# Kernel tuning notes

Measured on AMD Instinct MI355X. Metric: run time of the kernel, lower is better.

The kernel has to match this reference:

```python
import jax, jax.numpy as jnp
import numpy as np

BETA = 1.0  # config.beta
B, G, K, E2 = 1024, 512, 128, 128


def setup_inputs() -> dict:
    key = jax.random.key(0)
    k1, k2, k3, k4, k5 = jax.random.split(key, 5)
    s = 0.05
    return {
        "images": jax.random.normal(k1, (B, G), dtype=jnp.float32),
        "wimg": jax.random.normal(k2, (G, K), dtype=jnp.float32) * s,    # project.weight.T
        "wrec": jax.random.normal(k3, (K, E2), dtype=jnp.float32) * s,   # rec.weight.T
        "wrec2": jax.random.normal(k4, (K + 1, E2), dtype=jnp.float32) * s,  # rec2.weight.T
        "wimg2": jax.random.normal(k5, (G, K, K + 1), dtype=jnp.float32) * s,  # img2.weight.T.reshape(K+1,K,G).T
    }


def _soft_assign(x, codes):
    # x: [B, D], codes: [D, C] -> softmax over C of -beta * mean_D (x - codes)^2
    xh = -jnp.mean((x[:, :, None] - codes[None]) ** 2, axis=1) * BETA  # [B, C]
    return jax.nn.softmax(xh, axis=-1)


def reference(images, wimg, wrec, wrec2, wimg2):
    # ---- encode ----
    xp = _soft_assign(images, wimg)            # [B, K]
    lat = xp @ wrec                            # [B, E2]
    xp = _soft_assign(lat, wrec.T)             # [B, K] (codes are wrec.T: [E2, K])
    idx = jnp.argmax(xp, axis=-1)              # [B] hard component
    xwimg = jnp.transpose(wimg2[:, idx, :], (1, 0, 2))   # [B, G, K+1]
    base = wimg[:, idx].T[:, :, None]                     # [B, G, 1]
    xd = images[:, :, None] - base - xwimg                # [B, G, K+1]
    xh2 = -jnp.mean(xd ** 2, axis=1) * BETA               # [B, K+1]
    xp2 = jax.nn.softmax(xh2, axis=-1)
    lat2 = xp2 @ wrec2                                    # [B, E2]
    # ---- decode (ret='rec', n_step>=1) ----
    xp_d = _soft_assign(lat, wrec.T)           # [B, K]
    xp2_d = _soft_assign(lat2, wrec2.T)        # [B, K+1]
    wimgg = wimg[:, :, None] + wimg2           # [G, K, K+1]
    # tensordot(xp_d[:, :, None]*xp2_d[:, None, :], wimgg.permute(1,2,0), 2)
    xrec = jnp.einsum('bk,bj,gkj->bg', xp_d, xp2_d, wimgg)  # [B, G]
    # ---- loss ----
    loss = jnp.mean((xrec - images) ** 2, axis=-1)  # [B]
    return loss
```

## Files before the change

### kernel.cpp

```cpp
#include <hip/hip_runtime.h>

#define B_    1024
#define G_    512
#define K_    128
#define J_    129
#define JP_   132
#define E2_   128
#define KK_   16512
#define KK2_  16896
#define KKE2_ 17024
#define KKP_  17408
#define SPLITS 16
#define KCHUNK 1088
#define BK_   32
#define KSTEPS 34
#define GS_   8

using short8 = __attribute__((ext_vector_type(8))) short;
using f32x4  = __attribute__((ext_vector_type(4))) float;

__device__ __forceinline__ float bf2f(unsigned short h){
  return __uint_as_float(((unsigned int)h) << 16);
}
__device__ __forceinline__ unsigned short f2bf(float f){
  unsigned int u = __float_as_uint(f);
  u += 0x7fffu + ((u >> 16) & 1u);
  return (unsigned short)(u >> 16);
}

#define GLOAD16(gptr, ldst) __builtin_amdgcn_global_load_lds( \
    (const __attribute__((address_space(1))) unsigned int*)(gptr), \
    (__attribute__((address_space(3))) unsigned int*)(ldst), 16, 0, 0)

__device__ __forceinline__ float blockSum512(float v, float* red, int t){
  #pragma unroll
  for (int off = 32; off > 0; off >>= 1) v += __shfl_down(v, off);
  __syncthreads();
  if ((t & 63) == 0) red[t >> 6] = v;
  __syncthreads();
  float r = ((red[0] + red[1]) + (red[2] + red[3]))
          + ((red[4] + red[5]) + (red[6] + red[7]));
  __syncthreads();
  return r;
}

__device__ __forceinline__ void blockSoftmaxMS512(float x, bool act,
    float* redm, float* reds, int t, float& mo, float& so){
  float m = x, s = act ? 1.f : 0.f;
  #pragma unroll
  for (int off = 32; off > 0; off >>= 1){
    float om = __shfl_down(m, off);
    float os = __shfl_down(s, off);
    float nm = fmaxf(m, om);
    s = s*__expf(m - nm) + os*__expf(om - nm);
    m = nm;
  }
  __syncthreads();
  if ((t & 63) == 0){ redm[t >> 6] = m; reds[t >> 6] = s; }
  __syncthreads();
  float gm = redm[0], gsv = reds[0];
  #pragma unroll
  for (int w = 1; w < 8; w++){
    float om = redm[w], os = reds[w];
    float nm = fmaxf(gm, om);
    gsv = gsv*__expf(gm - nm) + os*__expf(om - nm);
    gm = nm;
  }
  mo = gm; so = gsv;
}

__device__ __forceinline__ int blockSoftmaxMSI512(float x, int idx, bool act,
    float* redm, float* reds, int* redi, int t, float& mo, float& so){
  float m = x, s = act ? 1.f : 0.f; int i = idx;
  #pragma unroll
  for (int off = 32; off > 0; off >>= 1){
    float om = __shfl_down(m, off);
    float os = __shfl_down(s, off);
    int   oi = __shfl_down(i, off);
    bool take = (om > m) || (om == m && oi < i);
    float nm = fmaxf(m, om);
    s = s*__expf(m - nm) + os*__expf(om - nm);
    i = take ? oi : i;
    m = nm;
  }
  __syncthreads();
  if ((t & 63) == 0){ redm[t >> 6] = m; reds[t >> 6] = s; redi[t >> 6] = i; }
  __syncthreads();
  float gm = redm[0], gsv = reds[0]; int gi = redi[0];
  #pragma unroll
  for (int w = 1; w < 8; w++){
    float om = redm[w], os = reds[w]; int oi = redi[w];
    bool take = (om > gm) || (om == gm && oi < gi);
    float nm = fmaxf(gm, om);
    gsv = gsv*__expf(gm - nm) + os*__expf(om - nm);
    gi = take ? oi : gi;
    gm = nm;
  }
  mo = gm; so = gsv;
  return gi;
}

__global__ __launch_bounds__(1024) void norms_kernel(
    const float* __restrict__ wimg, const float* __restrict__ wrec,
    const float* __restrict__ wrec2, float* __restrict__ c1norm,
    float* __restrict__ w3norm, float* __restrict__ w6norm,
    float* __restrict__ wrecT, float* __restrict__ wrec2T){
  int t = threadIdx.x;
  if (blockIdx.x == 0){
    __shared__ float red[8][128];
    int k = t & 127, sl = t >> 7;
    float s = 0.f;
    int g0 = sl * (G_/8);
    for (int g = g0; g < g0 + G_/8; g++){
      float v = wimg[g*K_ + k]; s += v*v;
    }
    red[sl][k] = s;
    __syncthreads();
    if (t < 128){
      float r = 0.f;
      #pragma unroll
      for (int i = 0; i < 8; i++) r += red[i][t];
      c1norm[t] = r;
    }
  } else if (blockIdx.x == 1){
    int wave = t >> 6, lane = t & 63;
    for (int k = wave; k < K_; k += 16){
      float v0 = wrec[k*E2_ + lane], v1 = wrec[k*E2_ + 64 + lane];
      float s = v0*v0 + v1*v1;
      #pragma unroll
      for (int off = 32; off > 0; off >>= 1) s += __shfl_down(s, off);
      if (lane == 0) w3norm[k] = s;
    }
  } else if (blockIdx.x == 2){
    int wave = t >> 6, lane = t & 63;
    for (int j = wave; j < J_; j += 16){
      float v0 = wrec2[j*E2_ + lane], v1 = wrec2[j*E2_ + 64 + lane];
      float s = v0*v0 + v1*v1;
      #pragma unroll
      for (int off = 32; off > 0; off >>= 1) s += __shfl_down(s, off);
      if (lane == 0) w6norm[j] = s;
    }
  } else if (blockIdx.x == 3){
    for (int n = t; n < K_*E2_; n += 1024){
      int k = n >> 7, e = n & 127;
      wrecT[e*K_ + k] = wrec[n];
    }
  } else {
    for (int n = t; n < J_*E2_; n += 1024){
      int j = n >> 7, e = n & 127;
      wrec2T[e*J_ + j] = wrec2[n];
    }
  }
}

__global__ __launch_bounds__(128) void tables_part_kernel(
    const float* __restrict__ wimg2, const float* __restrict__ wimg,
    float* __restrict__ sqp, float* __restrict__ crp,
    unsigned short* __restrict__ W2){
  int n  = blockIdx.x * 128 + threadIdx.x;
  int gs = blockIdx.y;
  int k = n / J_;
  int w2i = n + 3*k;
  float s0=0,s1=0,s2=0,s3=0, c0=0,c1=0,c2=0,c3=0;
  int gbase = gs * (G_/GS_);
  #pragma unroll 2
  for (int g = gbase; g < gbase + G_/GS_; g += 4){
    float w0 = wimg2[(size_t)(g  )*KK_ + n];
    float w1 = wimg2[(size_t)(g+1)*KK_ + n];
    float w2 = wimg2[(size_t)(g+2)*KK_ + n];
    float w3 = wimg2[(size_t)(g+3)*KK_ + n];
    W2[(size_t)(g  )*KKP_ + w2i] = f2bf(w0);
    W2[(size_t)(g+1)*KKP_ + w2i] = f2bf(w1);
    W2[(size_t)(g+2)*KKP_ + w2i] = f2bf(w2);
    W2[(size_t)(g+3)*KKP_ + w2i] = f2bf(w3);
    s0 += w0*w0; s1 += w1*w1; s2 += w2*w2; s3 += w3*w3;
    c0 += wimg[(g  )*K_ + k]*w0;
    c1 += wimg[(g+1)*K_ + k]*w1;
    c2 += wimg[(g+2)*K_ + k]*w2;
    c3 += wimg[(g+3)*K_ + k]*w3;
  }
  sqp[(size_t)gs*KK_ + n] = (s0+s1)+(s2+s3);
  crp[(size_t)gs*KK_ + n] = (c0+c1)+(c2+c3);
}
__global__ __launch_bounds__(128) void tables_reduce_kernel(
    const float* __restrict__ sqp, const float* __restrict__ crp,
    float* __restrict__ sq2, float* __restrict__ cross){
  int n = blockIdx.x * 128 + threadIdx.x;
  float s = 0.f, c = 0.f;
  #pragma unroll
  for (int gs = 0; gs < GS_; gs++){
    s += sqp[(size_t)gs*KK_ + n];
    c += crp[(size_t)gs*KK_ + n];
  }
  sq2[n] = s; cross[n] = c;
}

__global__ __launch_bounds__(128) void w2tail_kernel(
    const float* __restrict__ wimg, unsigned short* __restrict__ W2){
  int g = blockIdx.x, t = threadIdx.x;
  unsigned short* dst = W2 + (size_t)g * KKP_;
  dst[KK2_ + t]        = f2bf(wimg[g*K_ + t]);
  dst[KKE2_ + t]       = 0;
  dst[KKE2_ + 128 + t] = 0;
  dst[KKE2_ + 256 + t] = 0;
  dst[t*JP_ + 129] = 0;
  dst[t*JP_ + 130] = 0;
  dst[t*JP_ + 131] = 0;
}

__global__ __launch_bounds__(512, 8) void encdec_kernel(
    const float* __restrict__ img,  const float* __restrict__ wimg,
    const float* __restrict__ wrec, const float* __restrict__ wrec2,
    const float* __restrict__ wrecT, const float* __restrict__ wrec2T,
    const unsigned short* __restrict__ W2,
    const float* __restrict__ c1norm, const float* __restrict__ w3norm,
    const float* __restrict__ w6norm, const float* __restrict__ sq2,
    const float* __restrict__ cross, unsigned short* __restrict__ Rm){
  __shared__ __align__(16) float simg[G_];
  __shared__ float sp[K_];
  __shared__ float sqv[J_];
  __shared__ float slat[E2_];
  __shared__ float sd1[K_];
  __shared__ __align__(16) float sh16[16][128];
  __shared__ float sh4[4][K_];
  __shared__ float xtra[2];
  __shared__ float redm[8], reds[8];
  __shared__ int   redi[8];

  int t = threadIdx.x;
  int b = blockIdx.x;
  int tt = t & 127, q = t >> 7;
  int ll = t & 31, gq = t >> 5;

  simg[t] = img[b*G_ + t];
  __syncthreads();
  float a0 = simg[t];
  float imgnorm = blockSum512(a0*a0, redm, t);

  {
    float p0=0,p1=0,p2=0,p3=0;
    int g0 = gq * 32;
    #pragma unroll 4
    for (int g = g0; g < g0 + 32; g++){
      float4 wv = *(const float4*)(wimg + g*K_ + 4*ll);
      float sv = simg[g];
      p0 += sv*wv.x; p1 += sv*wv.y; p2 += sv*wv.z; p3 += sv*wv.w;
    }
    float4 st = {p0, p1, p2, p3};
    *(float4*)&sh16[gq][4*ll] = st;
  }
  __syncthreads();
  float xh1 = -3e38f, d1 = 0.f;
  if (t < 128){
    #pragma unroll
    for (int i = 0; i < 16; i++) d1 += sh16[i][t];
    sd1[t] = d1;
    xh1 = -(imgnorm - 2.f*d1 + c1norm[t]) * (1.f/512.f);
  }
  float m1, s1;
  blockSoftmaxMS512(xh1, t < 128, redm, reds, t, m1, s1);
  if (t < 128) sp[t] = __expf(xh1 - m1) / s1;
  __syncthreads();

  {
    float l0=0,l1=0;
    int k0 = q * 32;
    for (int k = k0; k < k0 + 32; k += 2){
      l0 += sp[k  ] * wrec[(k  )*E2_ + tt];
      l1 += sp[k+1] * wrec[(k+1)*E2_ + tt];
    }
    sh4[q][tt] = l0 + l1;
  }
  __syncthreads();
  float lat = (sh4[0][tt] + sh4[1][tt]) + (sh4[2][tt] + sh4[3][tt]);
  if (q == 0) slat[tt] = lat;
  float latnorm = blockSum512((q == 0) ? lat*lat : 0.f, redm, t);

  {
    float l0=0,l1=0;
    int e0 = q * 32;
    const float* rT = wrecT + tt;
    for (int e = e0; e < e0 + 32; e += 2){
      l0 += slat[e  ] * rT[(e  )*K_];
      l1 += slat[e+1] * rT[(e+1)*K_];
    }
    sh4[q][tt] = l0 + l1;
  }
  __syncthreads();
  float xh3 = -3e38f;
  if (t < 128){
    float d3 = (sh4[0][t] + sh4[1][t]) + (sh4[2][t] + sh4[3][t]);
    xh3 = -(latnorm - 2.f*d3 + w3norm[t]) * (1.f/128.f);
  }
  float m3, s3;
  int idxb = blockSoftmaxMSI512(xh3, tt, t < 128, redm, reds, redi, t, m3, s3);
  if (t < 128) sp[t] = __expf(xh3 - m3) / s3;
  float dsq = imgnorm - 2.f*sd1[idxb] + c1norm[idxb];

  {
    const unsigned short* Wb = W2 + (size_t)idxb * JP_ + 4*ll;
    float p0=0,p1=0,p2=0,p3=0;
    int g0 = gq * 32;
    #pragma unroll 4
    for (int g = g0; g < g0 + 32; g++){
      uint2 wv = *(const uint2*)(Wb + (size_t)g*KKP_);
      float sv = simg[g];
      p0 += sv * __uint_as_float(wv.x << 16);
      p1 += sv * __uint_as_float(wv.x & 0xffff0000u);
      p2 += sv * __uint_as_float(wv.y << 16);
      p3 += sv * __uint_as_float(wv.y & 0xffff0000u);
    }
    float4 st = {p0, p1, p2, p3};
    *(float4*)&sh16[gq][4*ll] = st;
  }
  if (t < 64){
    const unsigned short* Wb8 = W2 + (size_t)idxb * JP_ + 128;
    float s = 0.f;
    #pragma unroll
    for (int m = 0; m < 8; m++){
      int g = t + 64*m;
      s += simg[g] * bf2f(Wb8[(size_t)g * KKP_]);
    }
    #pragma unroll
    for (int off = 32; off > 0; off >>= 1) s += __shfl_down(s, off);
    if (t == 0) xtra[0] = s;
  }
  __syncthreads();
  float xh2 = -3e38f;
  if (t < J_){
    float di;
    if (t < 128){
      di = 0.f;
      #pragma unroll
      for (int i = 0; i < 16; i++) di += sh16[i][t];
    } else di = xtra[0];
    int nb = idxb*J_ + t;
    xh2 = -(dsq - 2.f*(di - cross[nb]) + sq2[nb]) * (1.f/512.f);
  }
  float m2, s2;
  blockSoftmaxMS512(xh2, t < J_, redm, reds, t, m2, s2);
  if (t < J_) sqv[t] = __expf(xh2 - m2) / s2;
  __syncthreads();

  {
    float lv = 0.f;
    int j0 = (q == 0) ? 0 : (q*32 + 1);
    int j1 = q*32 + 33;
    for (int j = j0; j < j1; j++)
      lv += sqv[j] * wrec2[j*E2_ + tt];
    sh4[q][tt] = lv;
  }
  __syncthreads();
  float lat2 = (sh4[0][tt] + sh4[1][tt]) + (sh4[2][tt] + sh4[3][tt]);
  if (q == 0) slat[tt] = lat2;
  float l2n = blockSum512((q == 0) ? lat2*lat2 : 0.f, redm, t);

  {
    float l0=0,l1=0;
    int e0 = q * 32;
    const float* rT = wrec2T + tt;
    for (int e = e0; e < e0 + 32; e += 2){
      l0 += slat[e  ] * rT[(e  )*J_];
      l1 += slat[e+1] * rT[(e+1)*J_];
    }
    sh4[q][tt] = l0 + l1;
  }
  if (t < 64){
    float s = slat[t]*wrec2T[t*J_ + 128] + slat[t+64]*wrec2T[(t+64)*J_ + 128];
    #pragma unroll
    for (int off = 32; off > 0; off >>= 1) s += __shfl_down(s, off);
    if (t == 0) xtra[1] = s;
  }
  __syncthreads();
  float xh6 = -3e38f;
  if (t < J_){
    float d6 = (t < 128) ? ((sh4[0][t] + sh4[1][t]) + (sh4[2][t] + sh4[3][t])) : xtra[1];
    xh6 = -(l2n - 2.f*d6 + w6norm[t]) * (1.f/128.f);
  }
  float m6, s6;
  blockSoftmaxMS512(xh6, t < J_, redm, reds, t, m6, s6);
  if (t < J_) sqv[t] = __expf(xh6 - m6) / s6;
  __syncthreads();

  unsigned short* Rrow = Rm + (size_t)b * KKP_;
  int k = t / JP_;
  int j = t - k*JP_;
  for (int kk = t; kk < KKP_; kk += 512){
    float v = 0.f;
    if (kk < KK2_){
      if (j < J_) v = sp[k] * sqv[j];
    } else if (kk < KKE2_) v = sp[kk - KK2_];
    Rrow[kk] = f2bf(v);
    j += 116;
    if (j >= JP_){ j -= JP_; k += 4; } else k += 3;
  }
}

__global__ __launch_bounds__(256) void gemm_kernel(
    const unsigned short* __restrict__ Rm, const unsigned short* __restrict__ W2,
    float* __restrict__ part){
  __shared__ __align__(16) unsigned int lds[4096];
  unsigned int* lA = lds;
  unsigned int* lB = lds + 2048;
  auto lA3 = (__attribute__((address_space(3))) unsigned int*)lA;
  auto lB3 = (__attribute__((address_space(3))) unsigned int*)lB;
  int tid = threadIdx.x;
  int l = tid & 63;
  int wv = tid >> 6;
  int wr = (wv >> 1) * 64, wc = (wv & 1) * 64;
  int b0 = blockIdx.y * 128, g0 = blockIdx.x * 128;
  size_t kkbase = (size_t)blockIdx.z * KCHUNK;

  int srow = tid >> 2, scol = tid & 3;
  const unsigned short* ga  = Rm + (size_t)(b0 + srow)*KKP_ + kkbase + scol*8;
  const unsigned short* ga2 = ga + (size_t)64 * KKP_;
  const unsigned short* gb  = W2 + (size_t)(g0 + srow)*KKP_ + kkbase + scol*8;
  const unsigned short* gb2 = gb + (size_t)64 * KKP_;

  int lrow = l & 15, lko = (l >> 4) << 2;

  f32x4 zero4 = {0.f, 0.f, 0.f, 0.f};
  f32x4 acc[4][4];
  #pragma unroll
  for (int mi = 0; mi < 4; mi++)
    #pragma unroll
    for (int ni = 0; ni < 4; ni++) acc[mi][ni] = zero4;

  for (int s = 0; s < KSTEPS; s++){
    __syncthreads();
    GLOAD16(ga,  lA3 + wv*256);
    GLOAD16(ga2, lA3 + 1024 + wv*256);
    GLOAD16(gb,  lB3 + wv*256);
    GLOAD16(gb2, lB3 + 1024 + wv*256);
    ga += BK_; ga2 += BK_; gb += BK_; gb2 += BK_;
    __syncthreads();
    short8 af[4], bfv[4];
    #pragma unroll
    for (int mi = 0; mi < 4; mi++)
      af[mi] = *(const short8*)(lA + (wr + mi*16 + lrow)*16 + lko);
    #pragma unroll
    for (int ni = 0; ni < 4; ni++)
      bfv[ni] = *(const short8*)(lB + (wc + ni*16 + lrow)*16 + lko);
    #pragma unroll
    for (int mi = 0; mi < 4; mi++)
      #pragma unroll
      for (int ni = 0; ni < 4; ni++)
        acc[mi][ni] = __builtin_amdgcn_mfma_f32_16x16x32_bf16(af[mi], bfv[ni], acc[mi][ni], 0, 0, 0);
  }

  float* P = part + ((size_t)blockIdx.z * B_ + b0) * G_ + g0;
  int rh = (l >> 4) << 2, cl = l & 15;
  #pragma unroll
  for (int mi = 0; mi < 4; mi++)
    #pragma unroll
    for (int ni = 0; ni < 4; ni++)
      #pragma unroll
      for (int r = 0; r < 4; r++){
        int row = wr + mi*16 + rh + r;
        int col = wc + ni*16 + cl;
        P[(size_t)row*G_ + col] = acc[mi][ni][r];
      }
}

__global__ __launch_bounds__(128) void loss_kernel(
    const float* __restrict__ img, const float* __restrict__ part,
    float* __restrict__ out){
  __shared__ float redf[2];
  int t = threadIdx.x, b = blockIdx.x;
  float acc = 0.f;
  for (int g = t; g < G_; g += 128){
    float x = 0.f;
    #pragma unroll
    for (int z = 0; z < SPLITS; z++)
      x += part[((size_t)z*B_ + b)*G_ + g];
    float d = x - img[b*G_ + g];
    acc += d*d;
  }
  #pragma unroll
  for (int off = 32; off > 0; off >>= 1) acc += __shfl_down(acc, off);
  __syncthreads();
  if ((t & 63) == 0) redf[t >> 6] = acc;
  __syncthreads();
  if (t == 0) out[b] = (redf[0] + redf[1]) * (1.f/512.f);
}

extern "C" void kernel_launch(void* const* d_in, const int* in_sizes, int n_in,
                              void* d_out, int out_size, void* d_ws, size_t ws_size,
                              hipStream_t stream){
  (void)in_sizes; (void)n_in; (void)out_size; (void)ws_size;
  const float* img   = (const float*)d_in[0];
  const float* wimg  = (const float*)d_in[1];
  const float* wrec  = (const float*)d_in[2];
  const float* wrec2 = (const float*)d_in[3];
  const float* wimg2 = (const float*)d_in[4];
  float* out = (float*)d_out;

  char* ws = (char*)d_ws;
  size_t off = 0;
  auto alloc = [&](size_t bytes) -> void* {
    void* p = ws + off;
    off += (bytes + 255) & ~(size_t)255;
    return p;
  };
  unsigned short* W2   = (unsigned short*)alloc((size_t)G_ * KKP_ * 2);
  unsigned short* Rm   = (unsigned short*)alloc((size_t)B_ * KKP_ * 2);
  float* part   = (float*)alloc((size_t)SPLITS * B_ * G_ * 4);
  float* sqp    = (float*)alloc((size_t)GS_ * KK_ * 4);
  float* crp    = (float*)alloc((size_t)GS_ * KK_ * 4);
  float* sq2    = (float*)alloc((size_t)KK_ * 4);
  float* cross  = (float*)alloc((size_t)KK_ * 4);
  float* c1norm = (float*)alloc(K_ * 4);
  float* w3norm = (float*)alloc(K_ * 4);
  float* w6norm = (float*)alloc(J_ * 4);
  float* wrecT  = (float*)alloc((size_t)K_ * E2_ * 4);
  float* wrec2T = (float*)alloc((size_t)J_ * E2_ * 4);

  norms_kernel<<<dim3(5), dim3(1024), 0, stream>>>(wimg, wrec, wrec2, c1norm, w3norm, w6norm, wrecT, wrec2T);
  tables_part_kernel<<<dim3(129, GS_), dim3(128), 0, stream>>>(wimg2, wimg, sqp, crp, W2);
  tables_reduce_kernel<<<dim3(129), dim3(128), 0, stream>>>(sqp, crp, sq2, cross);
  w2tail_kernel<<<dim3(512), dim3(128), 0, stream>>>(wimg, W2);
  encdec_kernel<<<dim3(1024), dim3(512), 0, stream>>>(img, wimg, wrec, wrec2, wrecT, wrec2T, W2,
      c1norm, w3norm, w6norm, sq2, cross, Rm);
  gemm_kernel<<<dim3(4, 8, SPLITS), dim3(256), 0, stream>>>(Rm, W2, part);
  loss_kernel<<<dim3(1024), dim3(128), 0, stream>>>(img, part, out);
}
```

Measured before the change: 126.9 us.

## Double-buffer LDS tiles in bf16 GEMM and pack R-matrix stores as pairs

The GEMM kernel now uses two LDS buffers. The next K-slice's global-to-LDS loads are issued before the MFMAs on the current slice, and the second barrier per iteration is dropped, so memory latency can overlap compute. The R-row builder now writes two bf16 values per 32-bit store instead of one 16-bit store per element, which halves store instructions. The cost is double the LDS footprint per block (32 KB), which may reduce occupancy, and the design relies on the top-of-loop barrier waiting for the outstanding async loads.

Measured after the change: 122.9 us. 3.1% less time.

```diff
diff --git a/kernel.cpp b/kernel.cpp
--- a/kernel.cpp
+++ b/kernel.cpp
@@ -382,28 +382,31 @@
   if (t < J_) sqv[t] = __expf(xh6 - m6) / s6;
   __syncthreads();
 
-  unsigned short* Rrow = Rm + (size_t)b * KKP_;
-  int k = t / JP_;
-  int j = t - k*JP_;
-  for (int kk = t; kk < KKP_; kk += 512){
-    float v = 0.f;
-    if (kk < KK2_){
-      if (j < J_) v = sp[k] * sqv[j];
-    } else if (kk < KKE2_) v = sp[kk - KK2_];
-    Rrow[kk] = f2bf(v);
-    j += 116;
-    if (j >= JP_){ j -= JP_; k += 4; } else k += 3;
+  unsigned int* Rrow32 = (unsigned int*)(Rm + (size_t)b * KKP_);
+  int k = t / 66;
+  int j2 = t - k*66;
+  for (int kk2 = t; kk2 < KKP_/2; kk2 += 512){
+    float v0 = 0.f, v1 = 0.f;
+    if (kk2 < KK2_/2){
+      int j = 2*j2;
+      float pk = sp[k];
+      v0 = (j   < J_) ? pk * sqv[j]   : 0.f;
+      v1 = (j+1 < J_) ? pk * sqv[j+1] : 0.f;
+    } else if (kk2 < KKE2_/2){
+      int e = 2*(kk2 - KK2_/2);
+      v0 = sp[e]; v1 = sp[e+1];
+    }
+    Rrow32[kk2] = (unsigned int)f2bf(v0) | ((unsigned int)f2bf(v1) << 16);
+    j2 += 50;
+    if (j2 >= 66){ j2 -= 66; k += 8; } else k += 7;
   }
 }
 
 __global__ __launch_bounds__(256) void gemm_kernel(
     const unsigned short* __restrict__ Rm, const unsigned short* __restrict__ W2,
     float* __restrict__ part){
-  __shared__ __align__(16) unsigned int lds[4096];
-  unsigned int* lA = lds;
-  unsigned int* lB = lds + 2048;
-  auto lA3 = (__attribute__((address_space(3))) unsigned int*)lA;
-  auto lB3 = (__attribute__((address_space(3))) unsigned int*)lB;
+  __shared__ __align__(16) unsigned int lds[8192];
+  auto lds3 = (__attribute__((address_space(3))) unsigned int*)lds;
   int tid = threadIdx.x;
   int l = tid & 63;
   int wv = tid >> 6;
@@ -426,14 +429,25 @@
     #pragma unroll
     for (int ni = 0; ni < 4; ni++) acc[mi][ni] = zero4;
 
+  GLOAD16(ga,  lds3 + wv*256);
+  GLOAD16(ga2, lds3 + 1024 + wv*256);
+  GLOAD16(gb,  lds3 + 2048 + wv*256);
+  GLOAD16(gb2, lds3 + 3072 + wv*256);
+  ga += BK_; ga2 += BK_; gb += BK_; gb2 += BK_;
+
+  int cur = 0;
   for (int s = 0; s < KSTEPS; s++){
     __syncthreads();
-    GLOAD16(ga,  lA3 + wv*256);
-    GLOAD16(ga2, lA3 + 1024 + wv*256);
-    GLOAD16(gb,  lB3 + wv*256);
-    GLOAD16(gb2, lB3 + 1024 + wv*256);
-    ga += BK_; ga2 += BK_; gb += BK_; gb2 += BK_;
-    __syncthreads();
+    if (s + 1 < KSTEPS){
+      unsigned int nb = (cur ^ 1) * 4096;
+      GLOAD16(ga,  lds3 + nb + wv*256);
+      GLOAD16(ga2, lds3 + nb + 1024 + wv*256);
+      GLOAD16(gb,  lds3 + nb + 2048 + wv*256);
+      GLOAD16(gb2, lds3 + nb + 3072 + wv*256);
+      ga += BK_; ga2 += BK_; gb += BK_; gb2 += BK_;
+    }
+    const unsigned int* lA = lds + cur*4096;
+    const unsigned int* lB = lA + 2048;
     short8 af[4], bfv[4];
     #pragma unroll
     for (int mi = 0; mi < 4; mi++)
@@ -446,6 +460,7 @@
       #pragma unroll
       for (int ni = 0; ni < 4; ni++)
         acc[mi][ni] = __builtin_amdgcn_mfma_f32_16x16x32_bf16(af[mi], bfv[ni], acc[mi][ni], 0, 0, 0);
+    cur ^= 1;
   }
 
   float* P = part + ((size_t)blockIdx.z * B_ + b0) * G_ + g0;
```
